# Kernel tuning notes

Hardware: AMD Instinct MI355X
Metric: run time of the kernel (lower is better)

The kernel has to match this reference:

```python
import jax, jax.numpy as jnp
import numpy as np

N_TOKENS = 16384
DIM = 4096
NUM_EXPERTS = 128
TOP_K = 8


def setup_inputs() -> dict:
    key = jax.random.key(0)
    k1, k2 = jax.random.split(key)
    x = jax.random.normal(k1, (N_TOKENS, DIM), dtype=jnp.float32)
    gate_w = jax.random.normal(k2, (NUM_EXPERTS, DIM), dtype=jnp.float32) * (DIM ** -0.5)
    return {"x": x, "gate_w": gate_w, "experts_per_token": TOP_K, "num_experts": NUM_EXPERTS}


def reference(x, gate_w, experts_per_token, num_experts):
    # gate: x @ W^T -> (N, E) logits
    scores = jnp.einsum('nd,ed->ne', x, gate_w)
    # softmax in fp32, cast back to input dtype
    probs = jax.nn.softmax(scores.astype(jnp.float32), axis=-1).astype(x.dtype)
    # stable descending argsort (argsort of negated probs, stable)
    sorted_indices = jnp.argsort(-probs, axis=1, stable=True)
    selected_experts = sorted_indices[:, :experts_per_token]            # (N, k)
    top_scores = jnp.take_along_axis(probs, selected_experts, axis=1)   # (N, k)
    # norm_topk_prob=True: renormalize selected weights to sum to 1
    denom = jnp.clip(top_scores.sum(axis=-1, keepdims=True), 1e-8, None)
    top_scores = top_scores / denom
    flat_experts = selected_experts.reshape(-1)                         # (N*k,)
    num_tokens_per_expert = jnp.bincount(flat_experts, length=num_experts)
    # stable sort token-slots by expert id for expert grouping
    perm = jnp.argsort(flat_experts, stable=True)                       # (N*k,)
    top_scores_sorted = top_scores.reshape(-1)[perm]
    token_indices = perm // experts_per_token
    return top_scores_sorted, token_indices, num_tokens_per_expert
```

## Files before the change

### kernel.cpp

```cpp
#include <hip/hip_runtime.h>
#include <math.h>

typedef _Float16 f16;
typedef f16 f16x8 __attribute__((ext_vector_type(8)));
typedef float f32x4 __attribute__((ext_vector_type(4)));

#define NT    16384
#define DIM   4096
#define NEXP  128
#define TOPK  8
#define NFLAT (NT * TOPK)
#define BT    32
#define NFB   (NT / BT)
#define SBLK  512
#define BK    64
#define NSTEP (DIM / BK)

#define COUNTS_OFF 0
#define SEL_OFF    1024
#define WGT_OFF    (SEL_OFF + NFLAT * 4)
#define BH_OFF     (WGT_OFF + NFLAT * 4)
#define BO_OFF     (BH_OFF + NEXP * SBLK * 4)
#define WPK_OFF    (BO_OFF + NEXP * SBLK * 4)

__device__ __forceinline__ void split2(float v, f16& h, f16& m) {
    h = (f16)v;
    m = (f16)((v - (float)h) * 2048.0f);
}

__global__ __launch_bounds__(256)
void wsplit_kernel(const float* __restrict__ gw, char* __restrict__ wpk) {
    const int t = blockIdx.x * 256 + threadIdx.x;
    const int l = t & 63, kkc = (t >> 6) & 1, g = (t >> 7) & 7, st = t >> 10;
    const int e = g * 16 + (l & 15);
    const int k0 = st * 64 + kkc * 32 + (l >> 4) * 8;
    float4 a = *(const float4*)&gw[e * 4096 + k0];
    float4 b = *(const float4*)&gw[e * 4096 + k0 + 4];
    union { f16 f[8]; uint4 u; } ph, pm;
    split2(a.x * 64.f, ph.f[0], pm.f[0]); split2(a.y * 64.f, ph.f[1], pm.f[1]);
    split2(a.z * 64.f, ph.f[2], pm.f[2]); split2(a.w * 64.f, ph.f[3], pm.f[3]);
    split2(b.x * 64.f, ph.f[4], pm.f[4]); split2(b.y * 64.f, ph.f[5], pm.f[5]);
    split2(b.z * 64.f, ph.f[6], pm.f[6]); split2(b.w * 64.f, ph.f[7], pm.f[7]);
    const size_t base = ((size_t)(st * 8 + g) * 4 + kkc) * 1024 + l * 16;
    *(uint4*)(wpk + base)        = ph.u;
    *(uint4*)(wpk + base + 2048) = pm.u;
}

__global__ __launch_bounds__(256, 3)
void fused_kernel(const float* __restrict__ x, const char* __restrict__ wpk,
                  float* __restrict__ wgt, int* __restrict__ sel,
                  int* __restrict__ counts, int* __restrict__ bh) {
    __shared__ __align__(16) char smem[17408];

    const int tid  = threadIdx.x;
    const int tok0 = blockIdx.x * BT;
    const int lane = tid & 63, eg = tid >> 6;
    const int fr = lane & 15, hi = lane >> 4;
    const int srow = tid >> 3;
    const int skq  = (tid & 7) * 8;
    const int xi = srow >> 4, xfr = srow & 15;
    const int xkk = skq >> 5, xhi = (skq >> 3) & 3;
    const int xslot = xhi * 16 + xfr;
    const int xwb = ((xi * 2 + xkk) * 64 + (xslot ^ ((xslot >> 4) << 1))) * 16;
    const int lxs = (lane ^ ((lane >> 4) << 1)) * 16;

    f32x4 acc0[2][2], acc1[2][2];
#pragma unroll
    for (int i = 0; i < 2; ++i)
#pragma unroll
        for (int j = 0; j < 2; ++j) {
            acc0[i][j] = (f32x4){0.f, 0.f, 0.f, 0.f};
            acc1[i][j] = (f32x4){0.f, 0.f, 0.f, 0.f};
        }

    const size_t xrow = (size_t)(tok0 + srow) * DIM;

#define X_PREF(RA, RB, SI) { \
    RA = *(const float4*)&x[xrow + (size_t)(SI) * BK + skq]; \
    RB = *(const float4*)&x[xrow + (size_t)(SI) * BK + skq + 4]; }
#define B_PREF(SI, BH_, BM_) { \
    const char* wsrc = wpk + ((size_t)(SI) * 8 + 2 * eg) * 4096 + lane * 16; \
    BH_[0][0] = *(const f16x8*)(wsrc); \
    BH_[0][1] = *(const f16x8*)(wsrc + 1024); \
    BM_[0][0] = *(const f16x8*)(wsrc + 2048); \
    BM_[0][1] = *(const f16x8*)(wsrc + 3072); \
    BH_[1][0] = *(const f16x8*)(wsrc + 4096); \
    BH_[1][1] = *(const f16x8*)(wsrc + 5120); \
    BM_[1][0] = *(const f16x8*)(wsrc + 6144); \
    BM_[1][1] = *(const f16x8*)(wsrc + 7168); }
#define STAGE(CUR, RA, RB) { \
    union { f16 f[8]; f16x8 v; } ph, pm; \
    split2(RA.x, ph.f[0], pm.f[0]); split2(RA.y, ph.f[1], pm.f[1]); \
    split2(RA.z, ph.f[2], pm.f[2]); split2(RA.w, ph.f[3], pm.f[3]); \
    split2(RB.x, ph.f[4], pm.f[4]); split2(RB.y, ph.f[5], pm.f[5]); \
    split2(RB.z, ph.f[6], pm.f[6]); split2(RB.w, ph.f[7], pm.f[7]); \
    *(f16x8*)(smem + (CUR) * 4096 + xwb) = ph.v; \
    *(f16x8*)(smem + 8192 + (CUR) * 4096 + xwb) = pm.v; }
#define COMPUTE(CUR, BH_, BM_) { \
    _Pragma("unroll") \
    for (int kk = 0; kk < 2; ++kk) { \
        f16x8 ah[2], am[2]; \
        _Pragma("unroll") \
        for (int i = 0; i < 2; ++i) { \
            const int xb = (CUR) * 4096 + (i * 2 + kk) * 1024 + lxs; \
            ah[i] = *(const f16x8*)(smem + xb); \
            am[i] = *(const f16x8*)(smem + 8192 + xb); \
        } \
        _Pragma("unroll") \
        for (int i = 0; i < 2; ++i) \
        _Pragma("unroll") \
        for (int j = 0; j < 2; ++j) { \
            acc0[i][j] = __builtin_amdgcn_mfma_f32_16x16x32_f16(ah[i], BH_[j][kk], acc0[i][j], 0, 0, 0); \
            acc1[i][j] = __builtin_amdgcn_mfma_f32_16x16x32_f16(ah[i], BM_[j][kk], acc1[i][j], 0, 0, 0); \
            acc1[i][j] = __builtin_amdgcn_mfma_f32_16x16x32_f16(am[i], BH_[j][kk], acc1[i][j], 0, 0, 0); \
        } \
    } }
#define STEP(CUR, RA, RB, BHU, BMU, BHP, BMP, PX, PB, SI) { \
    STAGE(CUR, RA, RB); \
    asm volatile("s_waitcnt lgkmcnt(0)" ::: "memory"); \
    __builtin_amdgcn_s_barrier(); \
    if (PX) { X_PREF(RA, RB, (SI) + 2); } \
    if (PB) { B_PREF((SI) + 1, BHP, BMP); } \
    __builtin_amdgcn_s_setprio(1); \
    COMPUTE(CUR, BHU, BMU); \
    __builtin_amdgcn_s_setprio(0); }

    f16x8 bhA[2][2], bmA[2][2], bhB[2][2], bmB[2][2];
    float4 a0, b0, a1, b1;
    B_PREF(0, bhA, bmA);
    X_PREF(a0, b0, 0);
    X_PREF(a1, b1, 1);

    for (int st = 0; st < 62; st += 2) {
        STEP(0, a0, b0, bhA, bmA, bhB, bmB, 1, 1, st);
        STEP(1, a1, b1, bhB, bmB, bhA, bmA, 1, 1, st + 1);
    }
    STEP(0, a0, b0, bhA, bmA, bhB, bmB, 0, 1, 62);
    STEP(1, a1, b1, bhB, bmB, bhA, bmA, 0, 0, 63);

    __syncthreads();

    float* S = (float*)smem;
    int*   h = (int*)(smem + 16512);
#pragma unroll
    for (int i = 0; i < 2; ++i)
#pragma unroll
        for (int j = 0; j < 2; ++j)
#pragma unroll
            for (int q = 0; q < 4; ++q) {
                int t = i * 16 + hi * 4 + q;
                int e = eg * 32 + j * 16 + fr;
                S[t * 129 + e] =
                    (acc0[i][j][q] + acc1[i][j][q] * (1.0f / 2048.0f)) * (1.0f / 64.0f);
            }
    if (tid < NEXP) h[tid] = 0;
    __syncthreads();

    if (tid < BT) {
        float bs[8]; int bi[8];
#pragma unroll
        for (int q = 0; q < 8; ++q) { bs[q] = -3.0e38f; bi[q] = 0; }
        for (int e = 0; e < NEXP; ++e) {
            float s = S[tid * 129 + e];
            if (s > bs[7]) {
                int pos = 7;
#pragma unroll
                for (int q = 6; q >= 0; q--) pos = (s > bs[q]) ? q : pos;
#pragma unroll
                for (int q = 7; q >= 1; q--) {
                    bool sh = (q > pos);
                    bs[q] = sh ? bs[q - 1] : bs[q];
                    bi[q] = sh ? bi[q - 1] : bi[q];
                }
#pragma unroll
                for (int q = 0; q < 8; q++)
                    if (q == pos) { bs[q] = s; bi[q] = e; }
            }
        }
        float m = bs[0], sum = 0.f, ex[8];
#pragma unroll
        for (int q = 0; q < 8; ++q) { ex[q] = expf(bs[q] - m); sum += ex[q]; }
        float inv = 1.f / fmaxf(sum, 1e-8f);
        const int tok = tok0 + tid;
#pragma unroll
        for (int q = 0; q < 8; ++q) {
            wgt[tok * TOPK + q] = ex[q] * inv;
            sel[tok * TOPK + q] = bi[q];
            atomicAdd(&h[bi[q]], 1);
        }
    }
    __syncthreads();
    if (tid < NEXP) {
        int c = h[tid];
        bh[tid * SBLK + blockIdx.x] = c;
        if (c) atomicAdd(&counts[tid], c);
    }
}

__global__ void scan_kernel(const int* __restrict__ bh, const int* __restrict__ counts,
                            int* __restrict__ bo, float* __restrict__ out) {
    const int e = blockIdx.x, tid = threadIdx.x;
    __shared__ int pre[NEXP];
    __shared__ int wsum[8];
    if (tid < NEXP) pre[tid] = counts[tid];
    __syncthreads();
#pragma unroll
    for (int d = 1; d < NEXP; d <<= 1) {
        int o = (tid < NEXP && tid >= d) ? pre[tid - d] : 0;
        __syncthreads();
        if (tid < NEXP) pre[tid] += o;
        __syncthreads();
    }
    const int gb = (e == 0) ? 0 : pre[e - 1];
    if (tid == 0) out[2 * NFLAT + e] = (float)counts[e];

    const int lane = tid & 63, wid = tid >> 6;
    int v = bh[e * SBLK + tid];
    int sc = v;
#pragma unroll
    for (int d = 1; d < 64; d <<= 1) {
        int o = __shfl_up(sc, d);
        sc += (lane >= d) ? o : 0;
    }
    if (lane == 63) wsum[wid] = sc;
    __syncthreads();
    int add = 0;
#pragma unroll
    for (int ww = 0; ww < 8; ww++) add += (ww < wid) ? wsum[ww] : 0;
    bo[e * SBLK + tid] = gb + sc - v + add;
}

__global__ void scatter_kernel(const int* __restrict__ sel, const float* __restrict__ wgt,
                               const int* __restrict__ bo, float* __restrict__ out) {
    const int tid = threadIdx.x, b = blockIdx.x;
    const int i = b * 256 + tid;
    const int e = sel[i];
    const int lane = tid & 63, wid = tid >> 6;
    unsigned long long m = ~0ull;
#pragma unroll
    for (int bit = 0; bit < 7; bit++) {
        unsigned long long bal = __ballot((e >> bit) & 1);
        m &= ((e >> bit) & 1) ? bal : ~bal;
    }
    unsigned long long lower = (lane == 0) ? 0ull : (~0ull >> (64 - lane));
    int wrank = __popcll(m & lower);

    __shared__ int wh_[4][NEXP];
    ((int*)wh_)[tid] = 0; ((int*)wh_)[tid + 256] = 0;
    __syncthreads();
    if (wrank == 0) wh_[wid][e] = __popcll(m);
    __syncthreads();
    int off = 0;
#pragma unroll
    for (int ww = 0; ww < 4; ww++) off += (ww < wid) ? wh_[ww][e] : 0;

    int pos = bo[e * SBLK + b] + off + wrank;
    out[pos] = wgt[i];
    out[NFLAT + pos] = (float)(i >> 3);
}

extern "C" void kernel_launch(void* const* d_in, const int* in_sizes, int n_in,
                              void* d_out, int out_size, void* d_ws, size_t ws_size,
                              hipStream_t stream) {
    const float* x  = (const float*)d_in[0];
    const float* gw = (const float*)d_in[1];
    float* out = (float*)d_out;
    char*  ws  = (char*)d_ws;

    int*   counts = (int*)(ws + COUNTS_OFF);
    int*   sel    = (int*)(ws + SEL_OFF);
    float* wgt    = (float*)(ws + WGT_OFF);
    int*   bh     = (int*)(ws + BH_OFF);
    int*   bo     = (int*)(ws + BO_OFF);
    char*  wpk    = ws + WPK_OFF;

    hipMemsetAsync(counts, 0, NEXP * sizeof(int), stream);

    wsplit_kernel<<<256, 256, 0, stream>>>(gw, wpk);
    fused_kernel<<<NFB, 256, 0, stream>>>(x, wpk, wgt, sel, counts, bh);
    scan_kernel<<<NEXP, 512, 0, stream>>>(bh, counts, bo, out);
    scatter_kernel<<<SBLK, 256, 0, stream>>>(sel, wgt, bo, out);
}
```

Baseline: 138.1 us.

## Split gate GEMM over K across waves and move top-k into separate kernel

```diff
diff --git a/kernel.cpp b/kernel.cpp
--- a/kernel.cpp
+++ b/kernel.cpp
@@ -10,11 +10,11 @@
 #define NEXP  128
 #define TOPK  8
 #define NFLAT (NT * TOPK)
-#define BT    32
-#define NFB   (NT / BT)
 #define SBLK  512
+#define KS    4
+#define KPER  (DIM / KS)
 #define BK    64
-#define NSTEP (DIM / BK)
+#define NST   (KPER / BK)
 
 #define COUNTS_OFF 0
 #define SEL_OFF    1024
@@ -22,6 +22,7 @@
 #define BH_OFF     (WGT_OFF + NFLAT * 4)
 #define BO_OFF     (BH_OFF + NEXP * SBLK * 4)
 #define WPK_OFF    (BO_OFF + NEXP * SBLK * 4)
+#define PART_OFF   (WPK_OFF + NEXP * DIM * 4)
 
 __device__ __forceinline__ void split2(float v, f16& h, f16& m) {
     h = (f16)v;
@@ -46,122 +47,135 @@
     *(uint4*)(wpk + base + 2048) = pm.u;
 }
 
-__global__ __launch_bounds__(256, 3)
-void fused_kernel(const float* __restrict__ x, const char* __restrict__ wpk,
-                  float* __restrict__ wgt, int* __restrict__ sel,
-                  int* __restrict__ counts, int* __restrict__ bh) {
-    __shared__ __align__(16) char smem[17408];
-
+__global__ __launch_bounds__(256, 2)
+void gemm_kernel(const float* __restrict__ x, const char* __restrict__ wpk,
+                 float* __restrict__ partial) {
     const int tid  = threadIdx.x;
-    const int tok0 = blockIdx.x * BT;
-    const int lane = tid & 63, eg = tid >> 6;
+    const int lane = tid & 63;
+    const int gw   = blockIdx.x * 4 + (tid >> 6);
+    const int ks   = gw & 3;
+    const int tok0 = (gw >> 2) * 32;
     const int fr = lane & 15, hi = lane >> 4;
-    const int srow = tid >> 3;
-    const int skq  = (tid & 7) * 8;
-    const int xi = srow >> 4, xfr = srow & 15;
-    const int xkk = skq >> 5, xhi = (skq >> 3) & 3;
-    const int xslot = xhi * 16 + xfr;
-    const int xwb = ((xi * 2 + xkk) * 64 + (xslot ^ ((xslot >> 4) << 1))) * 16;
-    const int lxs = (lane ^ ((lane >> 4) << 1)) * 16;
-
-    f32x4 acc0[2][2], acc1[2][2];
+
+    f32x4 acc0[2][8], acc1[2][8];
 #pragma unroll
     for (int i = 0; i < 2; ++i)
 #pragma unroll
-        for (int j = 0; j < 2; ++j) {
+        for (int j = 0; j < 8; ++j) {
             acc0[i][j] = (f32x4){0.f, 0.f, 0.f, 0.f};
             acc1[i][j] = (f32x4){0.f, 0.f, 0.f, 0.f};
         }
 
-    const size_t xrow = (size_t)(tok0 + srow) * DIM;
-
-#define X_PREF(RA, RB, SI) { \
-    RA = *(const float4*)&x[xrow + (size_t)(SI) * BK + skq]; \
-    RB = *(const float4*)&x[xrow + (size_t)(SI) * BK + skq + 4]; }
-#define B_PREF(SI, BH_, BM_) { \
-    const char* wsrc = wpk + ((size_t)(SI) * 8 + 2 * eg) * 4096 + lane * 16; \
-    BH_[0][0] = *(const f16x8*)(wsrc); \
-    BH_[0][1] = *(const f16x8*)(wsrc + 1024); \
-    BM_[0][0] = *(const f16x8*)(wsrc + 2048); \
-    BM_[0][1] = *(const f16x8*)(wsrc + 3072); \
-    BH_[1][0] = *(const f16x8*)(wsrc + 4096); \
-    BH_[1][1] = *(const f16x8*)(wsrc + 5120); \
-    BM_[1][0] = *(const f16x8*)(wsrc + 6144); \
-    BM_[1][1] = *(const f16x8*)(wsrc + 7168); }
-#define STAGE(CUR, RA, RB) { \
-    union { f16 f[8]; f16x8 v; } ph, pm; \
-    split2(RA.x, ph.f[0], pm.f[0]); split2(RA.y, ph.f[1], pm.f[1]); \
-    split2(RA.z, ph.f[2], pm.f[2]); split2(RA.w, ph.f[3], pm.f[3]); \
-    split2(RB.x, ph.f[4], pm.f[4]); split2(RB.y, ph.f[5], pm.f[5]); \
-    split2(RB.z, ph.f[6], pm.f[6]); split2(RB.w, ph.f[7], pm.f[7]); \
-    *(f16x8*)(smem + (CUR) * 4096 + xwb) = ph.v; \
-    *(f16x8*)(smem + 8192 + (CUR) * 4096 + xwb) = pm.v; }
-#define COMPUTE(CUR, BH_, BM_) { \
+    const float* xcell[4];
+#pragma unroll
+    for (int c = 0; c < 4; ++c) {
+        const int i_ = c >> 1, kk_ = c & 1;
+        xcell[c] = x + (size_t)(tok0 + i_ * 16 + fr) * DIM + ks * KPER + kk_ * 32 + hi * 8;
+    }
+    const char* bbase = wpk + (size_t)(ks * NST * 8) * 4096 + lane * 16;
+
+    float4 xr[4][2];
+    f16x8 ah[4], am[4];
+    f16x8 bh[2][2], bm[2][2];
+
+#define XLOAD(ST) { \
     _Pragma("unroll") \
-    for (int kk = 0; kk < 2; ++kk) { \
-        f16x8 ah[2], am[2]; \
-        _Pragma("unroll") \
-        for (int i = 0; i < 2; ++i) { \
-            const int xb = (CUR) * 4096 + (i * 2 + kk) * 1024 + lxs; \
-            ah[i] = *(const f16x8*)(smem + xb); \
-            am[i] = *(const f16x8*)(smem + 8192 + xb); \
-        } \
-        _Pragma("unroll") \
-        for (int i = 0; i < 2; ++i) \
-        _Pragma("unroll") \
-        for (int j = 0; j < 2; ++j) { \
-            acc0[i][j] = __builtin_amdgcn_mfma_f32_16x16x32_f16(ah[i], BH_[j][kk], acc0[i][j], 0, 0, 0); \
-            acc1[i][j] = __builtin_amdgcn_mfma_f32_16x16x32_f16(ah[i], BM_[j][kk], acc1[i][j], 0, 0, 0); \
-            acc1[i][j] = __builtin_amdgcn_mfma_f32_16x16x32_f16(am[i], BH_[j][kk], acc1[i][j], 0, 0, 0); \
-        } \
+    for (int c = 0; c < 4; ++c) { \
+        const float* p = xcell[c] + (size_t)(ST) * BK; \
+        xr[c][0] = *(const float4*)p; \
+        xr[c][1] = *(const float4*)(p + 4); \
     } }
-#define STEP(CUR, RA, RB, BHU, BMU, BHP, BMP, PX, PB, SI) { \
-    STAGE(CUR, RA, RB); \
-    asm volatile("s_waitcnt lgkmcnt(0)" ::: "memory"); \
-    __builtin_amdgcn_s_barrier(); \
-    if (PX) { X_PREF(RA, RB, (SI) + 2); } \
-    if (PB) { B_PREF((SI) + 1, BHP, BMP); } \
-    __builtin_amdgcn_s_setprio(1); \
-    COMPUTE(CUR, BHU, BMU); \
-    __builtin_amdgcn_s_setprio(0); }
-
-    f16x8 bhA[2][2], bmA[2][2], bhB[2][2], bmB[2][2];
-    float4 a0, b0, a1, b1;
-    B_PREF(0, bhA, bmA);
-    X_PREF(a0, b0, 0);
-    X_PREF(a1, b1, 1);
-
-    for (int st = 0; st < 62; st += 2) {
-        STEP(0, a0, b0, bhA, bmA, bhB, bmB, 1, 1, st);
-        STEP(1, a1, b1, bhB, bmB, bhA, bmA, 1, 1, st + 1);
-    }
-    STEP(0, a0, b0, bhA, bmA, bhB, bmB, 0, 1, 62);
-    STEP(1, a1, b1, bhB, bmB, bhA, bmA, 0, 0, 63);
-
-    __syncthreads();
-
-    float* S = (float*)smem;
-    int*   h = (int*)(smem + 16512);
+#define XCONV { \
+    _Pragma("unroll") \
+    for (int c = 0; c < 4; ++c) { \
+        union { f16 f[8]; f16x8 v; } ph, pm; \
+        split2(xr[c][0].x, ph.f[0], pm.f[0]); split2(xr[c][0].y, ph.f[1], pm.f[1]); \
+        split2(xr[c][0].z, ph.f[2], pm.f[2]); split2(xr[c][0].w, ph.f[3], pm.f[3]); \
+        split2(xr[c][1].x, ph.f[4], pm.f[4]); split2(xr[c][1].y, ph.f[5], pm.f[5]); \
+        split2(xr[c][1].z, ph.f[6], pm.f[6]); split2(xr[c][1].w, ph.f[7], pm.f[7]); \
+        ah[c] = ph.v; am[c] = pm.v; \
+    } }
+#define BLOAD(SLOT, IDX) { \
+    const char* p = bbase + (size_t)(IDX) * 4096; \
+    bh[SLOT][0] = *(const f16x8*)(p); \
+    bh[SLOT][1] = *(const f16x8*)(p + 1024); \
+    bm[SLOT][0] = *(const f16x8*)(p + 2048); \
+    bm[SLOT][1] = *(const f16x8*)(p + 3072); }
+
+    XLOAD(0);
+    BLOAD(0, 0);
+    BLOAD(1, 1);
+
+    for (int st = 0; st < NST; ++st) {
+        XCONV;
+        if (st + 1 < NST) XLOAD(st + 1);
+        __builtin_amdgcn_s_setprio(1);
+#pragma unroll
+        for (int j = 0; j < 8; ++j) {
+            const int sl = j & 1;
+#pragma unroll
+            for (int kk = 0; kk < 2; ++kk)
+#pragma unroll
+                for (int i = 0; i < 2; ++i) {
+                    acc0[i][j] = __builtin_amdgcn_mfma_f32_16x16x32_f16(ah[i * 2 + kk], bh[sl][kk], acc0[i][j], 0, 0, 0);
+                    acc1[i][j] = __builtin_amdgcn_mfma_f32_16x16x32_f16(ah[i * 2 + kk], bm[sl][kk], acc1[i][j], 0, 0, 0);
+                    acc1[i][j] = __builtin_amdgcn_mfma_f32_16x16x32_f16(am[i * 2 + kk], bh[sl][kk], acc1[i][j], 0, 0, 0);
+                }
+            if (j < 6) {
+                BLOAD(sl, st * 8 + j + 2);
+            } else if (st + 1 < NST) {
+                BLOAD(sl, (st + 1) * 8 + (j - 6));
+            }
+        }
+        __builtin_amdgcn_s_setprio(0);
+    }
+
+    float* pbase = partial + ((size_t)ks * NT + tok0) * NEXP;
 #pragma unroll
     for (int i = 0; i < 2; ++i)
 #pragma unroll
-        for (int j = 0; j < 2; ++j)
+        for (int j = 0; j < 8; ++j)
 #pragma unroll
             for (int q = 0; q < 4; ++q) {
-                int t = i * 16 + hi * 4 + q;
-                int e = eg * 32 + j * 16 + fr;
-                S[t * 129 + e] =
+                const int t = i * 16 + hi * 4 + q;
+                const int e = j * 16 + fr;
+                pbase[(size_t)t * NEXP + e] =
                     (acc0[i][j][q] + acc1[i][j][q] * (1.0f / 2048.0f)) * (1.0f / 64.0f);
             }
+}
+
+__global__ __launch_bounds__(256)
+void topk_kernel(const float* __restrict__ partial, float* __restrict__ wgt,
+                 int* __restrict__ sel, int* __restrict__ counts,
+                 int* __restrict__ bh) {
+    __shared__ float S[32][132];
+    __shared__ int h[NEXP];
+    const int tid = threadIdx.x;
+    const int tok0 = blockIdx.x * 32;
+    const int tok = tid >> 3, c = tid & 7;
+
+    f32x4 s0 = {0, 0, 0, 0}, s1 = {0, 0, 0, 0}, s2 = {0, 0, 0, 0}, s3 = {0, 0, 0, 0};
+#pragma unroll
+    for (int ksq = 0; ksq < KS; ++ksq) {
+        const float* p = partial + ((size_t)ksq * NT + tok0 + tok) * NEXP + c * 16;
+        s0 += *(const f32x4*)(p);
+        s1 += *(const f32x4*)(p + 4);
+        s2 += *(const f32x4*)(p + 8);
+        s3 += *(const f32x4*)(p + 12);
+    }
+    *(f32x4*)&S[tok][c * 16]      = s0;
+    *(f32x4*)&S[tok][c * 16 + 4]  = s1;
+    *(f32x4*)&S[tok][c * 16 + 8]  = s2;
+    *(f32x4*)&S[tok][c * 16 + 12] = s3;
     if (tid < NEXP) h[tid] = 0;
     __syncthreads();
 
-    if (tid < BT) {
+    if (tid < 32) {
         float bs[8]; int bi[8];
 #pragma unroll
         for (int q = 0; q < 8; ++q) { bs[q] = -3.0e38f; bi[q] = 0; }
         for (int e = 0; e < NEXP; ++e) {
-            float s = S[tid * 129 + e];
+            float s = S[tid][e];
             if (s > bs[7]) {
                 int pos = 7;
 #pragma unroll
@@ -181,19 +195,19 @@
 #pragma unroll
         for (int q = 0; q < 8; ++q) { ex[q] = expf(bs[q] - m); sum += ex[q]; }
         float inv = 1.f / fmaxf(sum, 1e-8f);
-        const int tok = tok0 + tid;
+        const int tok_g = tok0 + tid;
 #pragma unroll
         for (int q = 0; q < 8; ++q) {
-            wgt[tok * TOPK + q] = ex[q] * inv;
-            sel[tok * TOPK + q] = bi[q];
+            wgt[tok_g * TOPK + q] = ex[q] * inv;
+            sel[tok_g * TOPK + q] = bi[q];
             atomicAdd(&h[bi[q]], 1);
         }
     }
     __syncthreads();
     if (tid < NEXP) {
-        int c = h[tid];
-        bh[tid * SBLK + blockIdx.x] = c;
-        if (c) atomicAdd(&counts[tid], c);
+        int cc = h[tid];
+        bh[tid * SBLK + blockIdx.x] = cc;
+        if (cc) atomicAdd(&counts[tid], cc);
     }
 }
 
@@ -267,17 +281,19 @@
     float* out = (float*)d_out;
     char*  ws  = (char*)d_ws;
 
-    int*   counts = (int*)(ws + COUNTS_OFF);
-    int*   sel    = (int*)(ws + SEL_OFF);
-    float* wgt    = (float*)(ws + WGT_OFF);
-    int*   bh     = (int*)(ws + BH_OFF);
-    int*   bo     = (int*)(ws + BO_OFF);
-    char*  wpk    = ws + WPK_OFF;
+    int*   counts  = (int*)(ws + COUNTS_OFF);
+    int*   sel     = (int*)(ws + SEL_OFF);
+    float* wgt     = (float*)(ws + WGT_OFF);
+    int*   bh      = (int*)(ws + BH_OFF);
+    int*   bo      = (int*)(ws + BO_OFF);
+    char*  wpk     = ws + WPK_OFF;
+    float* partial = (float*)(ws + PART_OFF);
 
     hipMemsetAsync(counts, 0, NEXP * sizeof(int), stream);
 
     wsplit_kernel<<<256, 256, 0, stream>>>(gw, wpk);
-    fused_kernel<<<NFB, 256, 0, stream>>>(x, wpk, wgt, sel, counts, bh);
+    gemm_kernel<<<512, 256, 0, stream>>>(x, wpk, partial);
+    topk_kernel<<<512, 256, 0, stream>>>(partial, wgt, sel, counts, bh);
     scan_kernel<<<NEXP, 512, 0, stream>>>(bh, counts, bo, out);
     scatter_kernel<<<SBLK, 256, 0, stream>>>(sel, wgt, bo, out);
 }
```

New measurement: 157.6 us. +14.1%, slower.

## Stream gate weights via direct global-to-LDS loads and keep x in registers

Applied to the files above, without the earlier changes.

```diff
diff --git a/kernel.cpp b/kernel.cpp
--- a/kernel.cpp
+++ b/kernel.cpp
@@ -10,11 +10,10 @@
 #define NEXP  128
 #define TOPK  8
 #define NFLAT (NT * TOPK)
+#define SBLK  512
 #define BT    32
-#define NFB   (NT / BT)
-#define SBLK  512
 #define BK    64
-#define NSTEP (DIM / BK)
+#define NST   (DIM / BK)
 
 #define COUNTS_OFF 0
 #define SEL_OFF    1024
@@ -22,6 +21,14 @@
 #define BH_OFF     (WGT_OFF + NFLAT * 4)
 #define BO_OFF     (BH_OFF + NEXP * SBLK * 4)
 #define WPK_OFF    (BO_OFF + NEXP * SBLK * 4)
+
+#define G1P __attribute__((address_space(1)))
+#define L3P __attribute__((address_space(3)))
+
+__device__ __forceinline__ void gload_lds16(const void* g, void* l) {
+    __builtin_amdgcn_global_load_lds((const G1P unsigned int*)g,
+                                     (L3P unsigned int*)l, 16, 0, 0);
+}
 
 __device__ __forceinline__ void split2(float v, f16& h, f16& m) {
     h = (f16)v;
@@ -46,23 +53,16 @@
     *(uint4*)(wpk + base + 2048) = pm.u;
 }
 
-__global__ __launch_bounds__(256, 3)
+__global__ __launch_bounds__(256, 2)
 void fused_kernel(const float* __restrict__ x, const char* __restrict__ wpk,
                   float* __restrict__ wgt, int* __restrict__ sel,
                   int* __restrict__ counts, int* __restrict__ bh) {
-    __shared__ __align__(16) char smem[17408];
+    __shared__ __align__(16) char WB[65536];
 
     const int tid  = threadIdx.x;
     const int tok0 = blockIdx.x * BT;
     const int lane = tid & 63, eg = tid >> 6;
     const int fr = lane & 15, hi = lane >> 4;
-    const int srow = tid >> 3;
-    const int skq  = (tid & 7) * 8;
-    const int xi = srow >> 4, xfr = srow & 15;
-    const int xkk = skq >> 5, xhi = (skq >> 3) & 3;
-    const int xslot = xhi * 16 + xfr;
-    const int xwb = ((xi * 2 + xkk) * 64 + (xslot ^ ((xslot >> 4) << 1))) * 16;
-    const int lxs = (lane ^ ((lane >> 4) << 1)) * 16;
 
     f32x4 acc0[2][2], acc1[2][2];
 #pragma unroll
@@ -73,75 +73,75 @@
             acc1[i][j] = (f32x4){0.f, 0.f, 0.f, 0.f};
         }
 
-    const size_t xrow = (size_t)(tok0 + srow) * DIM;
-
-#define X_PREF(RA, RB, SI) { \
-    RA = *(const float4*)&x[xrow + (size_t)(SI) * BK + skq]; \
-    RB = *(const float4*)&x[xrow + (size_t)(SI) * BK + skq + 4]; }
-#define B_PREF(SI, BH_, BM_) { \
-    const char* wsrc = wpk + ((size_t)(SI) * 8 + 2 * eg) * 4096 + lane * 16; \
-    BH_[0][0] = *(const f16x8*)(wsrc); \
-    BH_[0][1] = *(const f16x8*)(wsrc + 1024); \
-    BM_[0][0] = *(const f16x8*)(wsrc + 2048); \
-    BM_[0][1] = *(const f16x8*)(wsrc + 3072); \
-    BH_[1][0] = *(const f16x8*)(wsrc + 4096); \
-    BH_[1][1] = *(const f16x8*)(wsrc + 5120); \
-    BM_[1][0] = *(const f16x8*)(wsrc + 6144); \
-    BM_[1][1] = *(const f16x8*)(wsrc + 7168); }
-#define STAGE(CUR, RA, RB) { \
-    union { f16 f[8]; f16x8 v; } ph, pm; \
-    split2(RA.x, ph.f[0], pm.f[0]); split2(RA.y, ph.f[1], pm.f[1]); \
-    split2(RA.z, ph.f[2], pm.f[2]); split2(RA.w, ph.f[3], pm.f[3]); \
-    split2(RB.x, ph.f[4], pm.f[4]); split2(RB.y, ph.f[5], pm.f[5]); \
-    split2(RB.z, ph.f[6], pm.f[6]); split2(RB.w, ph.f[7], pm.f[7]); \
-    *(f16x8*)(smem + (CUR) * 4096 + xwb) = ph.v; \
-    *(f16x8*)(smem + 8192 + (CUR) * 4096 + xwb) = pm.v; }
-#define COMPUTE(CUR, BH_, BM_) { \
-    _Pragma("unroll") \
-    for (int kk = 0; kk < 2; ++kk) { \
-        f16x8 ah[2], am[2]; \
+    const float* xcell = x + (size_t)(tok0 + fr) * DIM + hi * 8;
+    const char*  wsrc0 = wpk + (size_t)(2 * eg) * 4096 + lane * 16;
+    char* const  wdst0 = WB + 2 * eg * 4096;
+
+    float4 xr0[4][2], xr1[4][2];
+    f16x8 ah[4], am[4];
+
+#define XLOAD(XR, ST) { \
+    _Pragma("unroll") \
+    for (int c = 0; c < 4; ++c) { \
+        const float* p = xcell + (size_t)(c >> 1) * 16 * DIM + (c & 1) * 32 + (size_t)(ST) * BK; \
+        XR[c][0] = *(const float4*)p; \
+        XR[c][1] = *(const float4*)(p + 4); \
+    } }
+#define XCONV(XR) { \
+    _Pragma("unroll") \
+    for (int c = 0; c < 4; ++c) { \
+        union { f16 f[8]; f16x8 v; } ph, pm; \
+        split2(XR[c][0].x, ph.f[0], pm.f[0]); split2(XR[c][0].y, ph.f[1], pm.f[1]); \
+        split2(XR[c][0].z, ph.f[2], pm.f[2]); split2(XR[c][0].w, ph.f[3], pm.f[3]); \
+        split2(XR[c][1].x, ph.f[4], pm.f[4]); split2(XR[c][1].y, ph.f[5], pm.f[5]); \
+        split2(XR[c][1].z, ph.f[6], pm.f[6]); split2(XR[c][1].w, ph.f[7], pm.f[7]); \
+        ah[c] = ph.v; am[c] = pm.v; \
+    } }
+#define W_PREF(ST, B) { \
+    const char* ws = wsrc0 + (size_t)(ST) * 8 * 4096; \
+    char* wd = wdst0 + (B) * 32768; \
+    _Pragma("unroll") \
+    for (int c = 0; c < 8; ++c) gload_lds16(ws + c * 1024, wd + c * 1024); }
+#define COMPUTE(B) { \
+    _Pragma("unroll") \
+    for (int kk = 0; kk < 2; ++kk) \
+    _Pragma("unroll") \
+    for (int j = 0; j < 2; ++j) { \
+        const char* bp = WB + (B) * 32768 + (2 * eg + j) * 4096 + kk * 1024 + lane * 16; \
+        f16x8 bhf = *(const f16x8*)bp; \
+        f16x8 bmf = *(const f16x8*)(bp + 2048); \
         _Pragma("unroll") \
         for (int i = 0; i < 2; ++i) { \
-            const int xb = (CUR) * 4096 + (i * 2 + kk) * 1024 + lxs; \
-            ah[i] = *(const f16x8*)(smem + xb); \
-            am[i] = *(const f16x8*)(smem + 8192 + xb); \
-        } \
-        _Pragma("unroll") \
-        for (int i = 0; i < 2; ++i) \
-        _Pragma("unroll") \
-        for (int j = 0; j < 2; ++j) { \
-            acc0[i][j] = __builtin_amdgcn_mfma_f32_16x16x32_f16(ah[i], BH_[j][kk], acc0[i][j], 0, 0, 0); \
-            acc1[i][j] = __builtin_amdgcn_mfma_f32_16x16x32_f16(ah[i], BM_[j][kk], acc1[i][j], 0, 0, 0); \
-            acc1[i][j] = __builtin_amdgcn_mfma_f32_16x16x32_f16(am[i], BH_[j][kk], acc1[i][j], 0, 0, 0); \
+            acc0[i][j] = __builtin_amdgcn_mfma_f32_16x16x32_f16(ah[i * 2 + kk], bhf, acc0[i][j], 0, 0, 0); \
+            acc1[i][j] = __builtin_amdgcn_mfma_f32_16x16x32_f16(ah[i * 2 + kk], bmf, acc1[i][j], 0, 0, 0); \
+            acc1[i][j] = __builtin_amdgcn_mfma_f32_16x16x32_f16(am[i * 2 + kk], bhf, acc1[i][j], 0, 0, 0); \
         } \
     } }
-#define STEP(CUR, RA, RB, BHU, BMU, BHP, BMP, PX, PB, SI) { \
-    STAGE(CUR, RA, RB); \
-    asm volatile("s_waitcnt lgkmcnt(0)" ::: "memory"); \
-    __builtin_amdgcn_s_barrier(); \
-    if (PX) { X_PREF(RA, RB, (SI) + 2); } \
-    if (PB) { B_PREF((SI) + 1, BHP, BMP); } \
+#define STEP(XRC, PX, PW, SI, VMSTR) { \
+    XCONV(XRC); \
+    asm volatile("s_waitcnt vmcnt(" VMSTR ")" ::: "memory"); \
+    __builtin_amdgcn_sched_barrier(0); \
+    if (PW) { W_PREF((SI) + 1, ((SI) + 1) & 1); } \
+    if (PX) { XLOAD(XRC, (SI) + 2); } \
     __builtin_amdgcn_s_setprio(1); \
-    COMPUTE(CUR, BHU, BMU); \
+    COMPUTE((SI) & 1); \
     __builtin_amdgcn_s_setprio(0); }
 
-    f16x8 bhA[2][2], bmA[2][2], bhB[2][2], bmB[2][2];
-    float4 a0, b0, a1, b1;
-    B_PREF(0, bhA, bmA);
-    X_PREF(a0, b0, 0);
-    X_PREF(a1, b1, 1);
+    XLOAD(xr0, 0);
+    W_PREF(0, 0);
+    XLOAD(xr1, 1);
 
     for (int st = 0; st < 62; st += 2) {
-        STEP(0, a0, b0, bhA, bmA, bhB, bmB, 1, 1, st);
-        STEP(1, a1, b1, bhB, bmB, bhA, bmA, 1, 1, st + 1);
-    }
-    STEP(0, a0, b0, bhA, bmA, bhB, bmB, 0, 1, 62);
-    STEP(1, a1, b1, bhB, bmB, bhA, bmA, 0, 0, 63);
-
-    __syncthreads();
-
-    float* S = (float*)smem;
-    int*   h = (int*)(smem + 16512);
+        STEP(xr0, 1, 1, st, "8");
+        STEP(xr1, 1, 1, st + 1, "8");
+    }
+    STEP(xr0, 0, 1, 62, "8");
+    STEP(xr1, 0, 0, 63, "0");
+
+    __syncthreads();
+
+    float* S = (float*)WB;
+    int*   h = (int*)(WB + 17408);
 #pragma unroll
     for (int i = 0; i < 2; ++i)
 #pragma unroll
@@ -150,7 +150,7 @@
             for (int q = 0; q < 4; ++q) {
                 int t = i * 16 + hi * 4 + q;
                 int e = eg * 32 + j * 16 + fr;
-                S[t * 129 + e] =
+                S[t * 132 + e] =
                     (acc0[i][j][q] + acc1[i][j][q] * (1.0f / 2048.0f)) * (1.0f / 64.0f);
             }
     if (tid < NEXP) h[tid] = 0;
@@ -161,7 +161,7 @@
 #pragma unroll
         for (int q = 0; q < 8; ++q) { bs[q] = -3.0e38f; bi[q] = 0; }
         for (int e = 0; e < NEXP; ++e) {
-            float s = S[tid * 129 + e];
+            float s = S[tid * 132 + e];
             if (s > bs[7]) {
                 int pos = 7;
 #pragma unroll
@@ -277,7 +277,7 @@
     hipMemsetAsync(counts, 0, NEXP * sizeof(int), stream);
 
     wsplit_kernel<<<256, 256, 0, stream>>>(gw, wpk);
-    fused_kernel<<<NFB, 256, 0, stream>>>(x, wpk, wgt, sel, counts, bh);
+    fused_kernel<<<NT / BT, 256, 0, stream>>>(x, wpk, wgt, sel, counts, bh);
     scan_kernel<<<NEXP, 512, 0, stream>>>(bh, counts, bo, out);
     scatter_kernel<<<SBLK, 256, 0, stream>>>(sel, wgt, bo, out);
 }
```

After: 203.2 us. 1.47x slower.
